# Performance work log

Hardware: AMD Instinct MI355X
Metric: run time of the kernel (lower is better)

Reference implementation:

```python
import jax, jax.numpy as jnp
import numpy as np

B, N = 16384, 20
F = 128          # n_node_features = n_neighbors_features = embed_dim
T = 100          # time_dim
E = 128          # n_edge_features
H = 2            # n_head
OUT = 128        # output_dimension
KEY_DIM = F + T + E  # 356


def setup_inputs() -> dict:
    key = jax.random.key(0)
    ks = jax.random.split(key, 24)
    s = 0.02
    inp = {
        "src_node_features": jax.random.normal(ks[0], (B, F), jnp.float32),
        "neighbors_features": jax.random.normal(ks[1], (B, N, F), jnp.float32),
        "neighbors_time_features": jax.random.normal(ks[2], (B, N, T), jnp.float32),
        "edge_features": jax.random.normal(ks[3], (B, N, E), jnp.float32),
        "neighbors_padding_mask": jax.random.randint(ks[4], (B, N), 0, 2).astype(bool),
        "weights": jax.random.uniform(ks[5], (B, N), jnp.float32),
        # transform: Linear(key_dim -> F)
        "Wt": jax.random.normal(ks[6], (F, KEY_DIM), jnp.float32) * s,
        "bt": jnp.zeros((F,), jnp.float32),
        # MultiheadAttention projections (embed_dim = kdim = vdim = F)
        "Wq": jax.random.normal(ks[7], (F, F), jnp.float32) * s,
        "bq": jnp.zeros((F,), jnp.float32),
        "Wk": jax.random.normal(ks[8], (F, F), jnp.float32) * s,
        "bk": jnp.zeros((F,), jnp.float32),
        "Wv": jax.random.normal(ks[9], (F, F), jnp.float32) * s,
        "bv": jnp.zeros((F,), jnp.float32),
        "Wo": jax.random.normal(ks[10], (F, F), jnp.float32) * s,
        "bo": jnp.zeros((F,), jnp.float32),
        # MergeLayer: fc1(query_dim + F -> F), fc2(F -> OUT)
        "W1": jax.random.normal(ks[11], (F, F + F), jnp.float32) * s,
        "b1": jnp.zeros((F,), jnp.float32),
        "W2": jax.random.normal(ks[12], (OUT, F), jnp.float32) * s,
        "b2": jnp.zeros((OUT,), jnp.float32),
    }
    return inp


def _gat_forward(src, nbr, timef, edgef, w, mask,
                 Wt, bt, Wq, bq, Wk, bk, Wv, bv, Wo, bo, W1, b1, W2, b2):
    b, f = src.shape
    dh = f // H
    scale = 1.0 / jnp.sqrt(jnp.asarray(dh, src.dtype))
    # key = transform(cat([nbr, edge, time])) * weights  -> [B,N,F]
    k_in = jnp.concatenate([nbr, edgef, timef], axis=2)
    keyv = (jnp.einsum('bnk,fk->bnf', k_in, Wt) + bt) * w[:, :, None]
    # invalid-neighborhood fixup: rows fully padded get their first slot unmasked
    invalid = mask.all(axis=1, keepdims=True)           # [B,1]
    mask = mask.at[:, 0].set(jnp.where(invalid[:, 0], False, mask[:, 0]))
    # projections (query_len = 1)
    q = (src @ Wq.T + bq).reshape(b, H, dh)             # [B,H,dh]
    k = (keyv @ Wk.T + bk).reshape(b, N, H, dh)         # [B,N,H,dh]
    v = (keyv @ Wv.T + bv).reshape(b, N, H, dh)
    scores = jnp.einsum('bhd,bnhd->bhn', q, k) * scale  # [B,H,N]
    scores = jnp.where(mask[:, None, :], -jnp.inf, scores)
    attn = jax.nn.softmax(scores, axis=-1)
    ctx = jnp.einsum('bhn,bnhd->bhd', attn, v).reshape(b, f)
    out = ctx @ Wo.T + bo                               # [B,F]
    out = jnp.where(invalid, jnp.asarray(0.0, out.dtype), out)
    out = jax.nn.relu(out)
    # MergeLayer: fc2(relu(fc1(cat([attn_out, src]))))
    hmid = jax.nn.relu(jnp.concatenate([out, src], axis=1) @ W1.T + b1)
    return hmid @ W2.T + b2


def reference(src_node_features, neighbors_features, neighbors_time_features,
              edge_features, neighbors_padding_mask, weights,
              Wt, bt, Wq, bq, Wk, bk, Wv, bv, Wo, bo, W1, b1, W2, b2):
    return _gat_forward(src_node_features, neighbors_features,
                        neighbors_time_features, edge_features, weights,
                        neighbors_padding_mask,
                        Wt, bt, Wq, bq, Wk, bk, Wv, bv, Wo, bo, W1, b1, W2, b2)
```

## Files before the change

kernel.cpp:

```cpp
#include <hip/hip_runtime.h>
#include <math.h>

#define NN 20
#define FF 128
#define TT 100
#define EE 128
#define KD 356

typedef unsigned int u32;
typedef unsigned short u16;
typedef unsigned long long u64;
typedef __attribute__((ext_vector_type(4))) float f32x4;
typedef __attribute__((ext_vector_type(8))) short s16x8;

__device__ __forceinline__ u16 f2b(float f) {
    u32 u = __float_as_uint(f);
    u32 r = u + 0x7FFFu + ((u >> 16) & 1u);
    return (u16)(r >> 16);
}
__device__ __forceinline__ float b2f(u16 h) { return __uint_as_float(((u32)h) << 16); }
__device__ __forceinline__ float blo(u32 u){ return __uint_as_float(u << 16); }
__device__ __forceinline__ float bhi(u32 u){ return __uint_as_float(u & 0xFFFF0000u); }
__device__ __forceinline__ u32 pk2(float a, float b){ return (u32)f2b(a) | ((u32)f2b(b) << 16); }


__global__ void prep_fuse(const float* __restrict__ Wt, const float* __restrict__ bt,
                          const float* __restrict__ Wk, const float* __restrict__ Wv,
                          const u32* __restrict__ maskw,
                          float* __restrict__ wkt, float* __restrict__ wvt,
                          float* __restrict__ kfb, float* __restrict__ vfb, int* __restrict__ flagp)
{
    const int blk = blockIdx.x, t = threadIdx.x;
    if (blk < KD) {
        __shared__ float col[FF];
        col[t] = Wt[t * KD + blk];
        __syncthreads();
        float ak = 0.f, av = 0.f;
        for (int j = 0; j < FF; ++j) {
            float c = col[j];
            ak = fmaf(Wk[t * FF + j], c, ak);
            av = fmaf(Wv[t * FF + j], c, av);
        }
        wkt[blk * FF + t] = ak;
        wvt[blk * FF + t] = av;
    } else if (blk == KD) {
        float ak = 0.f, av = 0.f;
        for (int j = 0; j < FF; ++j) {
            float c = bt[j];
            ak = fmaf(Wk[t * FF + j], c, ak);
            av = fmaf(Wv[t * FF + j], c, av);
        }
        kfb[t] = ak; vfb[t] = av;
    } else {
        int any = 0;
        for (int i = t; i < 8192; i += 128) any |= (maskw[i] > 1u) ? 1 : 0;
        any = __any(any) ? 1 : 0;
        __shared__ int red[2];
        if ((t & 63) == 0) red[t >> 6] = any;
        __syncthreads();
        if (t == 0) *flagp = (red[0] | red[1]) ? 1 : 0;
    }
}

__global__ void prep_pack_v4(const float* __restrict__ wkt, const float* __restrict__ wvt,
                             const float* __restrict__ Wq, const float* __restrict__ Wo,
                             const float* __restrict__ W1, const float* __restrict__ W2,
                             u16* __restrict__ kvB, u16* __restrict__ wqI, u16* __restrict__ woI,
                             u16* __restrict__ w1I, u16* __restrict__ w2I)
{
    const int id = blockIdx.x * 256 + threadIdx.x;
    if (id < 196608) {
        int chunk = id >> 9, e = id & 511;
        int ln = e >> 3, ee = e & 7;
        int kt = chunk >> 4, nb = chunk & 15;
        int k = kt * 32 + (ln >> 4) * 8 + ee;
        int n = nb * 16 + (ln & 15);
        float v = 0.f;
        if (k < KD) v = (n < FF) ? wkt[k * FF + n] : wvt[k * FF + (n - FF)];
        kvB[id] = f2b(v);
    } else if (id < 215040) {
        int e = id - 196608; int rem = e % 9216;
        int n = rem / 72, kk = rem % 72; int k = (e / 9216) * 64 + kk;
        wqI[e] = f2b(kk < 64 ? Wq[n * FF + k] : 0.f);
    } else if (id < 233472) {
        int e = id - 215040; int rem = e % 9216;
        int n = rem / 72, kk = rem % 72; int k = (e / 9216) * 64 + kk;
        woI[e] = f2b(kk < 64 ? Wo[n * FF + k] : 0.f);
    } else if (id < 270336) {
        int e = id - 233472; int rem = e % 9216;
        int n = rem / 72, kk = rem % 72; int k = (e / 9216) * 64 + kk;
        w1I[e] = f2b(kk < 64 ? W1[n * 2 * FF + k] : 0.f);
    } else if (id < 288768) {
        int e = id - 270336; int rem = e % 9216;
        int n = rem / 72, kk = rem % 72; int k = (e / 9216) * 64 + kk;
        w2I[e] = f2b(kk < 64 ? W2[n * FF + k] : 0.f);
    }
}

__device__ __forceinline__ void loadA32(const float* __restrict__ nbr,
                                        const float* __restrict__ edg,
                                        const float* __restrict__ tmf,
                                        size_t r, int g, int kt, f32x4& v0, f32x4& v1)
{
    int c0 = g * 8;
    if (kt < 4) {
        const float* p = nbr + r * 128 + kt * 32 + c0;
        v0 = *(const f32x4*)p; v1 = *(const f32x4*)(p + 4);
    } else if (kt < 8) {
        const float* p = edg + r * 128 + (kt - 4) * 32 + c0;
        v0 = *(const f32x4*)p; v1 = *(const f32x4*)(p + 4);
    } else {
        int c = (kt - 8) * 32 + c0;
        const float* p = tmf + r * 100 + c;
        v0 = (c + 3 < 100) ? *(const f32x4*)p       : (f32x4){0.f,0.f,0.f,0.f};
        v1 = (c + 7 < 100) ? *(const f32x4*)(p + 4) : (f32x4){0.f,0.f,0.f,0.f};
    }
}

__global__ __launch_bounds__(512) void kv_attn_fused2(
    const float* __restrict__ nbr, const float* __restrict__ edg, const float* __restrict__ tmf,
    const float* __restrict__ wgt, const float* __restrict__ bk, const float* __restrict__ bv,
    const u16* __restrict__ kvB, const float* __restrict__ kfb, const float* __restrict__ vfb,
    const u16* __restrict__ Qg, const void* __restrict__ maskp, const int* __restrict__ flagp,
    u16* __restrict__ ctxout, unsigned char* __restrict__ flags)
{
    __shared__ __align__(16) u16 smem[20800];
    const int tid = threadIdx.x;
    const int lane = tid & 63, wave = tid >> 6;
    const int wn = wave;
    const int Mbase = blockIdx.x * 80;
    const int Bbase = blockIdx.x * 4;
    const int kg = lane >> 4, l16 = lane & 15;

    const bool stg = tid < 320;
    const int skg = (tid >> 4) & 3;
    const int srow = (tid >> 6) * 16 + (tid & 15);
    const size_t gr = (size_t)(Mbase + srow);

    f32x4 acc[5][2] = {};

    f32x4 pa0, pa1;
    if (stg) loadA32(nbr, edg, tmf, gr, skg, 0, pa0, pa1);
    s16x8 bc0 = *(const s16x8*)(kvB + (size_t)(wn * 2 + 0) * 512 + lane * 8);
    s16x8 bc1 = *(const s16x8*)(kvB + (size_t)(wn * 2 + 1) * 512 + lane * 8);
    if (stg)
        *(uint4*)(&smem[tid * 8]) = make_uint4(pk2(pa0.x,pa0.y), pk2(pa0.z,pa0.w),
                                               pk2(pa1.x,pa1.y), pk2(pa1.z,pa1.w));
    __syncthreads();

    #pragma unroll
    for (int kt = 0; kt < 12; ++kt) {
        const u16* curA = smem + (kt & 1) * 2560;
        u16* nxtA = (u16*)smem + ((kt + 1) & 1) * 2560;

        f32x4 na0, na1; s16x8 bn0, bn1;
        if (kt < 11) {
            if (stg) loadA32(nbr, edg, tmf, gr, skg, kt + 1, na0, na1);
            bn0 = *(const s16x8*)(kvB + (size_t)((kt + 1) * 16 + wn * 2 + 0) * 512 + lane * 8);
            bn1 = *(const s16x8*)(kvB + (size_t)((kt + 1) * 16 + wn * 2 + 1) * 512 + lane * 8);
        }
        s16x8 af[5];
        #pragma unroll
        for (int mt = 0; mt < 5; ++mt)
            af[mt] = *(const s16x8*)(&curA[(mt * 4 + kg) * 128 + l16 * 8]);
        #pragma unroll
        for (int mt = 0; mt < 5; ++mt) {
            acc[mt][0] = __builtin_amdgcn_mfma_f32_16x16x32_bf16(af[mt], bc0, acc[mt][0], 0, 0, 0);
            acc[mt][1] = __builtin_amdgcn_mfma_f32_16x16x32_bf16(af[mt], bc1, acc[mt][1], 0, 0, 0);
        }
        if (kt < 11) {
            if (stg)
                *(uint4*)(&nxtA[tid * 8]) = make_uint4(pk2(na0.x,na0.y), pk2(na0.z,na0.w),
                                                       pk2(na1.x,na1.y), pk2(na1.z,na1.w));
            bc0 = bn0; bc1 = bn1;
        }
        __syncthreads();
    }

    u16* kvls = smem;
    {
        const int rg = (lane >> 4) * 4;
        #pragma unroll
        for (int mt = 0; mt < 5; ++mt) {
            const int r0 = mt * 16 + rg;
            float w4v[4];
            #pragma unroll
            for (int i = 0; i < 4; ++i) w4v[i] = wgt[Mbase + r0 + i];
            #pragma unroll
            for (int nt = 0; nt < 2; ++nt) {
                const int c = wn * 32 + nt * 16 + l16;
                const float fb = (c < FF) ? kfb[c] : vfb[c - FF];
                const float bb = (c < FF) ? bk[c]  : bv[c - FF];
                #pragma unroll
                for (int i = 0; i < 4; ++i)
                    kvls[(r0 + i) * 260 + c] = f2b(fmaf(acc[mt][nt][i] + fb, w4v[i], bb));
            }
        }
    }
    __syncthreads();

    {
        const int lb = wave >> 1, h = wave & 1;
        const int brow = Bbase + lb;
        const int flagv = *flagp;
        bool mybit = false;
        if (lane < NN) {
            if (flagv) mybit = ((const unsigned char*)maskp)[brow * NN + lane] != 0;
            else       mybit = ((const int*)maskp)[brow * NN + lane] != 0;
        }
        u64 bal = __ballot(mybit);
        u32 mb = (u32)(bal & 0xFFFFFull);
        const bool invalid = (mb == 0xFFFFFu);
        if (invalid) mb &= ~1u;
        if (h == 0 && lane == 0) flags[brow] = invalid ? 1 : 0;

        float p = 0.f;
        {
            const int n = lane & 31;
            float s = -INFINITY;
            if (lane < 32 && n < NN) {
                const u16* kr = kvls + (lb * NN + n) * 260 + h * 64;
                const u16* qr = Qg + (size_t)brow * 128 + h * 64;
                float d = 0.f;
                #pragma unroll
                for (int dc = 0; dc < 16; ++dc) {
                    uint2 kw = *(const uint2*)(kr + dc * 4);
                    uint2 qw = *(const uint2*)(qr + dc * 4);
                    d = fmaf(blo(kw.x), blo(qw.x), d);  d = fmaf(bhi(kw.x), bhi(qw.x), d);
                    d = fmaf(blo(kw.y), blo(qw.y), d);  d = fmaf(bhi(kw.y), bhi(qw.y), d);
                }
                s = ((mb >> n) & 1u) ? -INFINITY : d * 0.125f;
            }
            float mx = s;
            #pragma unroll
            for (int off = 16; off; off >>= 1) mx = fmaxf(mx, __shfl_xor(mx, off, 32));
            float e = (lane < 32 && (lane & 31) < NN) ? expf(s - mx) : 0.f;
            float sum = e;
            #pragma unroll
            for (int off = 16; off; off >>= 1) sum += __shfl_xor(sum, off, 32);
            p = (lane < 32) ? e / sum : 0.f;
        }
        float cacc = 0.f;
        #pragma unroll
        for (int n2 = 0; n2 < NN; ++n2) {
            float pn = __shfl(p, n2);
            cacc = fmaf(pn, b2f(kvls[(lb * NN + n2) * 260 + 128 + h * 64 + lane]), cacc);
        }
        ctxout[(size_t)brow * 128 + h * 64 + lane] = f2b(cacc);
    }
}

#define GM_Q 0
#define GM_O 1
#define GM_H 2
#define GM_F 3

template<int MODE>
__global__ __launch_bounds__(256) void gemm_small(
    const void* __restrict__ Asrc, const float* __restrict__ Asrc2,
    const u16* __restrict__ Bimg, const float* __restrict__ bias,
    const unsigned char* __restrict__ flags, void* __restrict__ outp)
{
    __shared__ u16 lA[64 * 72];
    __shared__ u16 lB[128 * 72];
    const int tid = threadIdx.x;
    const int Mbase = blockIdx.x * 64;
    const int lane = tid & 63, wave = tid >> 6;
    const int wm = wave >> 1, wn = wave & 1;
    const int row = tid >> 2, cg = tid & 3;

    constexpr int KTILES = (MODE == GM_H) ? 4 : 2;
    f32x4 acc[2][4] = {};
    const size_t r = (size_t)(Mbase + row);

    for (int kt = 0; kt < KTILES; ++kt) {
        if (MODE == GM_Q || (MODE == GM_H && kt >= 2)) {
            const float* ap = (MODE == GM_Q)
                ? ((const float*)Asrc + r * 128 + kt * 64 + cg * 16)
                : (Asrc2 + r * 128 + (kt - 2) * 64 + cg * 16);
            f32x4 x0 = *(const f32x4*)ap,       x1 = *(const f32x4*)(ap + 4);
            f32x4 x2 = *(const f32x4*)(ap + 8), x3 = *(const f32x4*)(ap + 12);
            *(uint4*)(&lA[row * 72 + cg * 16])     = make_uint4(pk2(x0.x,x0.y), pk2(x0.z,x0.w), pk2(x1.x,x1.y), pk2(x1.z,x1.w));
            *(uint4*)(&lA[row * 72 + cg * 16 + 8]) = make_uint4(pk2(x2.x,x2.y), pk2(x2.z,x2.w), pk2(x3.x,x3.y), pk2(x3.z,x3.w));
        } else {
            const u16* ap = (const u16*)Asrc + r * 128 + kt * 64 + cg * 16;
            *(uint4*)(&lA[row * 72 + cg * 16])     = *(const uint4*)ap;
            *(uint4*)(&lA[row * 72 + cg * 16 + 8]) = *(const uint4*)(ap + 8);
        }
        for (int c = wave; c < 18; c += 4) {
            const char* g = (const char*)Bimg + (size_t)kt * 18432 + c * 1024 + lane * 16;
            char* l = (char*)lB + c * 1024;
            __builtin_amdgcn_global_load_lds((const __attribute__((address_space(1))) u32*)g,
                                             (__attribute__((address_space(3))) u32*)l, 16, 0, 0);
        }
        __syncthreads();
        #pragma unroll
        for (int ks = 0; ks < 2; ++ks) {
            int kk = ks * 32 + (lane >> 4) * 8;
            s16x8 a[2], b[4];
            #pragma unroll
            for (int mt = 0; mt < 2; ++mt)
                a[mt] = *(const s16x8*)(&lA[(wm * 32 + mt * 16 + (lane & 15)) * 72 + kk]);
            #pragma unroll
            for (int nt = 0; nt < 4; ++nt)
                b[nt] = *(const s16x8*)(&lB[(wn * 64 + nt * 16 + (lane & 15)) * 72 + kk]);
            #pragma unroll
            for (int mt = 0; mt < 2; ++mt)
                #pragma unroll
                for (int nt = 0; nt < 4; ++nt)
                    acc[mt][nt] = __builtin_amdgcn_mfma_f32_16x16x32_bf16(a[mt], b[nt], acc[mt][nt], 0, 0, 0);
        }
        __syncthreads();
    }

    #pragma unroll
    for (int mt = 0; mt < 2; ++mt) {
        #pragma unroll
        for (int nt = 0; nt < 4; ++nt) {
            int colg = wn * 64 + nt * 16 + (lane & 15);
            float bb = bias[colg];
            #pragma unroll
            for (int i = 0; i < 4; ++i) {
                int rg = Mbase + wm * 32 + mt * 16 + (lane >> 4) * 4 + i;
                float val = acc[mt][nt][i] + bb;
                if (MODE == GM_O) { if (flags[rg]) val = 0.f; val = fmaxf(val, 0.f); }
                if (MODE == GM_H) val = fmaxf(val, 0.f);
                if (MODE == GM_F) ((float*)outp)[(size_t)rg * 128 + colg] = val;
                else              ((u16*)outp)[(size_t)rg * 128 + colg] = f2b(val);
            }
        }
    }
}


__global__ void prep_pack_r2(const float* __restrict__ wkt, const float* __restrict__ wvt,
                             const float* __restrict__ Wq, const float* __restrict__ Wo,
                             const float* __restrict__ W1, const float* __restrict__ W2,
                             u16* __restrict__ bpack, u32* __restrict__ wq2, u32* __restrict__ wo2,
                             u32* __restrict__ w12, u32* __restrict__ w22)
{
    const int id = blockIdx.x * 256 + threadIdx.x;
    if (id < 98304) {
        int kt = id >> 14;
        int o  = id & 16383;
        int n  = o >> 6;
        int kk = (o & 63) ^ ((n & 7) << 3);
        int k  = kt * 64 + kk;
        float v = 0.f;
        if (k < KD) v = (n < FF) ? wkt[k * FF + n] : wvt[k * FF + (n - FF)];
        bpack[id] = f2b(v);
    } else if (id < 106496) {
        int e = id - 98304; int j = e >> 6, tt = e & 63;
        wq2[e] = (u32)f2b(Wq[tt * FF + j]) | ((u32)f2b(Wq[(tt + 64) * FF + j]) << 16);
    } else if (id < 114688) {
        int e = id - 106496; int j = e >> 6, tt = e & 63;
        wo2[e] = (u32)f2b(Wo[tt * FF + j]) | ((u32)f2b(Wo[(tt + 64) * FF + j]) << 16);
    } else if (id < 131072) {
        int e = id - 114688; int j = e >> 6, tt = e & 63;
        w12[e] = (u32)f2b(W1[tt * 2 * FF + j]) | ((u32)f2b(W1[(tt + 64) * 2 * FF + j]) << 16);
    } else if (id < 139264) {
        int e = id - 131072; int j = e >> 6, tt = e & 63;
        w22[e] = (u32)f2b(W2[tt * FF + j]) | ((u32)f2b(W2[(tt + 64) * FF + j]) << 16);
    }
}

__global__ __launch_bounds__(512) void kv_gemm_r2(
    const float* __restrict__ nbr, const float* __restrict__ edg, const float* __restrict__ tmf,
    const float* __restrict__ wgt, const float* __restrict__ bk, const float* __restrict__ bv,
    const u16* __restrict__ bpack, const float* __restrict__ kfb, const float* __restrict__ vfb,
    u16* __restrict__ kvout)
{
    __shared__ u16 lA[128 * 64];
    __shared__ u16 lB[256 * 64];
    const int tid = threadIdx.x;
    const int Mbase = blockIdx.x * 128;
    const int lane = tid & 63, wave = tid >> 6;
    const int wm = wave >> 2, wn = wave & 3;

    f32x4 acc[4][4] = {};
    const int rq = tid >> 4;
    const int cq = tid & 15;

    for (int kt = 0; kt < 6; ++kt) {
        #pragma unroll
        for (int i = 0; i < 4; ++i) {
            int row = rq + i * 32;
            size_t r = (size_t)(Mbase + row);
            f32x4 v;
            if (kt < 2)       v = *(const f32x4*)(nbr + r * 128 + kt * 64 + cq * 4);
            else if (kt < 4)  v = *(const f32x4*)(edg + r * 128 + (kt - 2) * 64 + cq * 4);
            else if (kt == 4) v = *(const f32x4*)(tmf + r * 100 + cq * 4);
            else if (cq < 9)  v = *(const f32x4*)(tmf + r * 100 + 64 + cq * 4);
            else              v = (f32x4){0.f, 0.f, 0.f, 0.f};
            int off = row * 64 + ((cq * 4) ^ ((row & 7) << 3));
            *(uint2*)(&lA[off]) = make_uint2(pk2(v.x, v.y), pk2(v.z, v.w));
        }
        #pragma unroll
        for (int i = 0; i < 4; ++i) {
            int boff = wave * 4096 + i * 1024;
            const char* g = (const char*)bpack + (size_t)kt * 32768 + boff + lane * 16;
            char* l = (char*)lB + boff;
            __builtin_amdgcn_global_load_lds((const __attribute__((address_space(1))) u32*)g,
                                             (__attribute__((address_space(3))) u32*)l, 16, 0, 0);
        }
        __syncthreads();
        #pragma unroll
        for (int ks = 0; ks < 2; ++ks) {
            int kk = ks * 32 + (lane >> 4) * 8;
            s16x8 a[4], b[4];
            #pragma unroll
            for (int mt = 0; mt < 4; ++mt) {
                int m = wm * 64 + mt * 16 + (lane & 15);
                a[mt] = *(const s16x8*)(&lA[m * 64 + (kk ^ ((m & 7) << 3))]);
            }
            #pragma unroll
            for (int nt = 0; nt < 4; ++nt) {
                int n = wn * 64 + nt * 16 + (lane & 15);
                b[nt] = *(const s16x8*)(&lB[n * 64 + (kk ^ ((n & 7) << 3))]);
            }
            #pragma unroll
            for (int mt = 0; mt < 4; ++mt)
                #pragma unroll
                for (int nt = 0; nt < 4; ++nt)
                    acc[mt][nt] = __builtin_amdgcn_mfma_f32_16x16x32_bf16(a[mt], b[nt], acc[mt][nt], 0, 0, 0);
        }
        __syncthreads();
    }

    #pragma unroll
    for (int mt = 0; mt < 4; ++mt) {
        float w4[4];
        #pragma unroll
        for (int i = 0; i < 4; ++i)
            w4[i] = wgt[Mbase + wm * 64 + mt * 16 + (lane >> 4) * 4 + i];
        #pragma unroll
        for (int nt = 0; nt < 4; ++nt) {
            int c = wn * 64 + nt * 16 + (lane & 15);
            float fb   = (c < FF) ? kfb[c] : vfb[c - FF];
            float bias = (c < FF) ? bk[c]  : bv[c - FF];
            #pragma unroll
            for (int i = 0; i < 4; ++i) {
                int rr = Mbase + wm * 64 + mt * 16 + (lane >> 4) * 4 + i;
                float val = fmaf(acc[mt][nt][i] + fb, w4[i], bias);
                kvout[(size_t)rr * 256 + c] = f2b(val);
            }
        }
    }
}

__global__ __launch_bounds__(64) void gat_attn_r2(
    const float* __restrict__ src, const void* __restrict__ maskp,
    const float* __restrict__ bq, const float* __restrict__ bo,
    const float* __restrict__ b1, const float* __restrict__ b2,
    const u16* __restrict__ kv, const u32* __restrict__ wq2, const u32* __restrict__ wo2,
    const u32* __restrict__ w12, const u32* __restrict__ w22,
    const int* __restrict__ flagp, float* __restrict__ out)
{
    const int b = blockIdx.x, t = threadIdx.x;
    __shared__ u16 kls[NN * 132];
    __shared__ float s_src[FF], s_q[FF], s_ctx[FF], s_out[FF], s_h[FF];
    __shared__ float s_sc[2 * NN];

    const int flag = *flagp;
    bool mybit = false;
    if (t < NN) {
        if (flag) mybit = ((const unsigned char*)maskp)[b * NN + t] != 0;
        else      mybit = ((const int*)maskp)[b * NN + t] != 0;
    }
    u64 bal = __ballot(mybit);
    u32 mb = (u32)(bal & 0xFFFFFull);
    const bool invalid = (mb == 0xFFFFFu);
    if (invalid) mb &= ~1u;

    s_src[t] = src[(size_t)b * FF + t];
    s_src[t + 64] = src[(size_t)b * FF + 64 + t];

    float v0[NN], v1[NN];
    #pragma unroll
    for (int n = 0; n < NN; ++n) {
        const u16* row = kv + ((size_t)b * NN + n) * 256;
        kls[n * 132 + t]      = row[t];
        kls[n * 132 + 64 + t] = row[64 + t];
        v0[n] = b2f(row[128 + t]);
        v1[n] = b2f(row[192 + t]);
    }
    __syncthreads();

    {
        float q0 = bq[t], q1 = bq[64 + t];
        for (int j = 0; j < FF; ++j) {
            u32 u = wq2[j * 64 + t];
            float sj = s_src[j];
            q0 = fmaf(blo(u), sj, q0);
            q1 = fmaf(bhi(u), sj, q1);
        }
        s_q[t] = q0; s_q[64 + t] = q1;
    }
    __syncthreads();

    if (t < 2 * NN) {
        int h = t / NN, n = t - (t / NN) * NN;
        const u16* kr = kls + n * 132 + h * 64;
        const float* qr = s_q + h * 64;
        float s = 0.f;
        #pragma unroll
        for (int d = 0; d < 64; ++d) s = fmaf(qr[d], b2f(kr[d]), s);
        s *= 0.125f;
        s_sc[t] = ((mb >> n) & 1u) ? -INFINITY : s;
    }
    __syncthreads();
    if (t < 2) {
        float mx = -INFINITY;
        for (int n = 0; n < NN; ++n) mx = fmaxf(mx, s_sc[t * NN + n]);
        float e[NN]; float sum = 0.f;
        for (int n = 0; n < NN; ++n) { e[n] = expf(s_sc[t * NN + n] - mx); sum += e[n]; }
        float inv = 1.f / sum;
        for (int n = 0; n < NN; ++n) s_sc[t * NN + n] = e[n] * inv;
    }
    __syncthreads();

    {
        float c0 = 0.f, c1 = 0.f;
        #pragma unroll
        for (int n = 0; n < NN; ++n) {
            c0 = fmaf(s_sc[n],      v0[n], c0);
            c1 = fmaf(s_sc[NN + n], v1[n], c1);
        }
        s_ctx[t] = c0; s_ctx[64 + t] = c1;
    }
    __syncthreads();

    {
        float o0 = bo[t], o1 = bo[64 + t];
        for (int j = 0; j < FF; ++j) {
            u32 u = wo2[j * 64 + t];
            float cj = s_ctx[j];
            o0 = fmaf(blo(u), cj, o0);
            o1 = fmaf(bhi(u), cj, o1);
        }
        if (invalid) { o0 = 0.f; o1 = 0.f; }
        o0 = fmaxf(o0, 0.f); o1 = fmaxf(o1, 0.f);
        s_out[t] = o0; s_out[64 + t] = o1;
    }
    __syncthreads();

    {
        float h0 = b1[t], h1 = b1[64 + t];
        for (int j = 0; j < FF; ++j) {
            u32 u = w12[j * 64 + t];
            float xj = s_out[j];
            h0 = fmaf(blo(u), xj, h0);
            h1 = fmaf(bhi(u), xj, h1);
        }
        for (int j = 0; j < FF; ++j) {
            u32 u = w12[(FF + j) * 64 + t];
            float xj = s_src[j];
            h0 = fmaf(blo(u), xj, h0);
            h1 = fmaf(bhi(u), xj, h1);
        }
        h0 = fmaxf(h0, 0.f); h1 = fmaxf(h1, 0.f);
        s_h[t] = h0; s_h[64 + t] = h1;
    }
    __syncthreads();

    {
        float f0 = b2[t], f1 = b2[64 + t];
        for (int j = 0; j < FF; ++j) {
            u32 u = w22[j * 64 + t];
            float hj = s_h[j];
            f0 = fmaf(blo(u), hj, f0);
            f1 = fmaf(bhi(u), hj, f1);
        }
        out[(size_t)b * FF + t] = f0;
        out[(size_t)b * FF + 64 + t] = f1;
    }
}


#define FB_WKT  0
#define FB_WVT  (FB_WKT + KD*FF)
#define FB_KB   (FB_WVT + KD*FF)
#define FB_VB   (FB_KB + FF)
#define FB_WQT  (FB_VB + FF)
#define FB_WOT  (FB_WQT + FF*FF)
#define FB_W1T  (FB_WOT + FF*FF)
#define FB_W2T  (FB_W1T + 2*FF*FF)
#define FB_FLAG (FB_W2T + FF*FF)

__global__ void gat_prep_fb(const float* __restrict__ Wt, const float* __restrict__ bt,
                            const float* __restrict__ Wq, const float* __restrict__ Wk,
                            const float* __restrict__ Wv, const float* __restrict__ Wo,
                            const float* __restrict__ W1, const float* __restrict__ W2,
                            const u32* __restrict__ maskw, float* __restrict__ ws)
{
    const int blk = blockIdx.x;
    const int t = threadIdx.x;
    if (blk < KD) {
        __shared__ float col[FF];
        col[t] = Wt[t * KD + blk];
        __syncthreads();
        float ak = 0.f, av = 0.f;
        for (int j = 0; j < FF; ++j) {
            float c = col[j];
            ak = fmaf(Wk[t * FF + j], c, ak);
            av = fmaf(Wv[t * FF + j], c, av);
        }
        ws[FB_WKT + blk * FF + t] = ak;
        ws[FB_WVT + blk * FF + t] = av;
    } else if (blk == KD) {
        float ak = 0.f, av = 0.f;
        for (int j = 0; j < FF; ++j) {
            float c = bt[j];
            ak = fmaf(Wk[t * FF + j], c, ak);
            av = fmaf(Wv[t * FF + j], c, av);
        }
        ws[FB_KB + t] = ak;
        ws[FB_VB + t] = av;
    } else if (blk == KD + 1) {
        int any = 0;
        for (int i = t; i < 8192; i += 128) any |= (maskw[i] > 1u) ? 1 : 0;
        any = __any(any) ? 1 : 0;
        __shared__ int red[2];
        if ((t & 63) == 0) red[t >> 6] = any;
        __syncthreads();
        if (t == 0) ((int*)ws)[FB_FLAG] = (red[0] | red[1]) ? 1 : 0;
    } else {
        int id = (blk - (KD + 2)) * 128 + t;
        if (id < FF * FF) {
            int k = id >> 7, f = id & 127;
            ws[FB_WQT + id] = Wq[f * FF + k];
        } else if (id < 2 * FF * FF) {
            int e = id - FF * FF; int k = e >> 7, f = e & 127;
            ws[FB_WOT + e] = Wo[f * FF + k];
        } else if (id < 4 * FF * FF) {
            int e = id - 2 * FF * FF; int j = e >> 7, f = e & 127;
            ws[FB_W1T + e] = W1[f * (2 * FF) + j];
        } else if (id < 5 * FF * FF) {
            int e = id - 4 * FF * FF; int k = e >> 7, f = e & 127;
            ws[FB_W2T + e] = W2[f * FF + k];
        }
    }
}

__global__ __launch_bounds__(64) void gat_main_fb(
    const float* __restrict__ src, const float* __restrict__ nbr,
    const float* __restrict__ tmf, const float* __restrict__ edg,
    const void* __restrict__ maskp, const float* __restrict__ wgt,
    const float* __restrict__ bq, const float* __restrict__ bk,
    const float* __restrict__ bv, const float* __restrict__ bo,
    const float* __restrict__ b1, const float* __restrict__ b2,
    const float* __restrict__ ws, float* __restrict__ out)
{
    const int b = blockIdx.x;
    const int t = threadIdx.x;
    __shared__ __align__(16) float kin[KD * NN];
    __shared__ float s_src[FF], s_q[FF], s_ctx[FF], s_out[FF], s_h[FF];
    __shared__ float s_w[NN], s_sc[2 * NN];

    const int flag = ((const int*)ws)[FB_FLAG];
    bool mybit = false;
    if (t < NN) {
        if (flag) mybit = ((const unsigned char*)maskp)[b * NN + t] != 0;
        else      mybit = ((const int*)maskp)[b * NN + t] != 0;
    }
    u64 bal = __ballot(mybit);
    u32 mb = (u32)(bal & 0xFFFFFull);
    const bool invalid = (mb == 0xFFFFFu);
    if (invalid) mb &= ~1u;

    s_src[t] = src[(size_t)b * FF + t];
    s_src[t + 64] = src[(size_t)b * FF + 64 + t];
    if (t < NN) s_w[t] = wgt[(size_t)b * NN + t];

    for (int idx = t; idx < NN * FF; idx += 64) {
        int n = idx >> 7, j = idx & 127;
        kin[j * NN + n]         = nbr[((size_t)b * NN + n) * FF + j];
        kin[(128 + j) * NN + n] = edg[((size_t)b * NN + n) * EE + j];
    }
    for (int idx = t; idx < NN * TT; idx += 64) {
        int n = idx / TT, j = idx - n * TT;
        kin[(256 + j) * NN + n] = tmf[((size_t)b * NN + n) * TT + j];
    }
    __syncthreads();

    const float* wkt = ws + FB_WKT;
    const float* wvt = ws + FB_WVT;
    float ak0[NN], ak1[NN], av0[NN], av1[NN];
#pragma unroll
    for (int n = 0; n < NN; ++n) { ak0[n] = 0.f; ak1[n] = 0.f; av0[n] = 0.f; av1[n] = 0.f; }
    for (int k = 0; k < KD; ++k) {
        float wk0 = wkt[k * FF + t],      wk1 = wkt[k * FF + 64 + t];
        float wv0 = wvt[k * FF + t],      wv1 = wvt[k * FF + 64 + t];
        const float4* cp = (const float4*)(kin + k * NN);
        float4 ca = cp[0], cb = cp[1], cc = cp[2], cd = cp[3], ce = cp[4];
        const float c[NN] = { ca.x, ca.y, ca.z, ca.w,  cb.x, cb.y, cb.z, cb.w,
                              cc.x, cc.y, cc.z, cc.w,  cd.x, cd.y, cd.z, cd.w,
                              ce.x, ce.y, ce.z, ce.w };
#pragma unroll
        for (int n = 0; n < NN; ++n) {
            ak0[n] = fmaf(wk0, c[n], ak0[n]);
            ak1[n] = fmaf(wk1, c[n], ak1[n]);
            av0[n] = fmaf(wv0, c[n], av0[n]);
            av1[n] = fmaf(wv1, c[n], av1[n]);
        }
    }
    __syncthreads();

    float* kls = kin;
    float* vls = kin + NN * 129;
    {
        const float kb0 = ws[FB_KB + t], kb1 = ws[FB_KB + 64 + t];
        const float vb0 = ws[FB_VB + t], vb1 = ws[FB_VB + 64 + t];
        const float k0b = bk[t], k1b = bk[64 + t];
        const float v0b = bv[t], v1b = bv[64 + t];
#pragma unroll
        for (int n = 0; n < NN; ++n) {
            float wn = s_w[n];
            kls[n * 129 + t]      = fmaf(wn, ak0[n] + kb0, k0b);
            kls[n * 129 + 64 + t] = fmaf(wn, ak1[n] + kb1, k1b);
            vls[n * 129 + t]      = fmaf(wn, av0[n] + vb0, v0b);
            vls[n * 129 + 64 + t] = fmaf(wn, av1[n] + vb1, v1b);
        }
    }
    {
        const float* wqT = ws + FB_WQT;
        float q0 = bq[t], q1 = bq[64 + t];
        for (int j = 0; j < FF; ++j) {
            float sj = s_src[j];
            q0 = fmaf(wqT[j * FF + t], sj, q0);
            q1 = fmaf(wqT[j * FF + 64 + t], sj, q1);
        }
        s_q[t] = q0; s_q[64 + t] = q1;
    }
    __syncthreads();

    if (t < 2 * NN) {
        int h = t / NN, n = t - (t / NN) * NN;
        const float* kr = kls + n * 129 + h * 64;
        const float* qr = s_q + h * 64;
        float s = 0.f;
#pragma unroll
        for (int d = 0; d < 64; ++d) s = fmaf(qr[d], kr[d], s);
        s *= 0.125f;
        s_sc[t] = ((mb >> n) & 1u) ? -INFINITY : s;
    }
    __syncthreads();
    if (t < 2) {
        float mx = -INFINITY;
        for (int n = 0; n < NN; ++n) mx = fmaxf(mx, s_sc[t * NN + n]);
        float e[NN]; float sum = 0.f;
        for (int n = 0; n < NN; ++n) { e[n] = expf(s_sc[t * NN + n] - mx); sum += e[n]; }
        float inv = 1.f / sum;
        for (int n = 0; n < NN; ++n) s_sc[t * NN + n] = e[n] * inv;
    }
    __syncthreads();

    {
        float c0 = 0.f, c1 = 0.f;
#pragma unroll
        for (int n = 0; n < NN; ++n) {
            c0 = fmaf(s_sc[n],      vls[n * 129 + t],      c0);
            c1 = fmaf(s_sc[NN + n], vls[n * 129 + 64 + t], c1);
        }
        s_ctx[t] = c0; s_ctx[64 + t] = c1;
    }
    __syncthreads();

    {
        const float* woT = ws + FB_WOT;
        float o0 = bo[t], o1 = bo[64 + t];
        for (int j = 0; j < FF; ++j) {
            float cj = s_ctx[j];
            o0 = fmaf(woT[j * FF + t], cj, o0);
            o1 = fmaf(woT[j * FF + 64 + t], cj, o1);
        }
        if (invalid) { o0 = 0.f; o1 = 0.f; }
        o0 = fmaxf(o0, 0.f); o1 = fmaxf(o1, 0.f);
        s_out[t] = o0; s_out[64 + t] = o1;
    }
    __syncthreads();

    {
        const float* w1T = ws + FB_W1T;
        float h0 = b1[t], h1 = b1[64 + t];
        for (int j = 0; j < FF; ++j) {
            float xj = s_out[j];
            h0 = fmaf(w1T[j * FF + t], xj, h0);
            h1 = fmaf(w1T[j * FF + 64 + t], xj, h1);
        }
        for (int j = 0; j < FF; ++j) {
            float xj = s_src[j];
            h0 = fmaf(w1T[(FF + j) * FF + t], xj, h0);
            h1 = fmaf(w1T[(FF + j) * FF + 64 + t], xj, h1);
        }
        h0 = fmaxf(h0, 0.f); h1 = fmaxf(h1, 0.f);
        s_h[t] = h0; s_h[64 + t] = h1;
    }
    __syncthreads();

    {
        const float* w2T = ws + FB_W2T;
        float f0 = b2[t], f1 = b2[64 + t];
        for (int j = 0; j < FF; ++j) {
            float hj = s_h[j];
            f0 = fmaf(w2T[j * FF + t], hj, f0);
            f1 = fmaf(w2T[j * FF + 64 + t], hj, f1);
        }
        out[(size_t)b * FF + t] = f0;
        out[(size_t)b * FF + 64 + t] = f1;
    }
}


extern "C" void kernel_launch(void* const* d_in, const int* in_sizes, int n_in,
                              void* d_out, int out_size, void* d_ws, size_t ws_size,
                              hipStream_t stream)
{
    const float* src = (const float*)d_in[0];
    const float* nbr = (const float*)d_in[1];
    const float* tmf = (const float*)d_in[2];
    const float* edg = (const float*)d_in[3];
    const void*  msk = d_in[4];
    const float* wgt = (const float*)d_in[5];
    const float* Wt  = (const float*)d_in[6];
    const float* bt  = (const float*)d_in[7];
    const float* Wq  = (const float*)d_in[8];
    const float* bq  = (const float*)d_in[9];
    const float* Wk  = (const float*)d_in[10];
    const float* bk  = (const float*)d_in[11];
    const float* Wv  = (const float*)d_in[12];
    const float* bv  = (const float*)d_in[13];
    const float* Wo  = (const float*)d_in[14];
    const float* bo  = (const float*)d_in[15];
    const float* W1  = (const float*)d_in[16];
    const float* b1  = (const float*)d_in[17];
    const float* W2  = (const float*)d_in[18];
    const float* b2  = (const float*)d_in[19];

    const int B = in_sizes[0] / FF;
    const size_t M = (size_t)B * NN;

    size_t o1 = 0;
    size_t t1_qa   = o1; o1 += (size_t)B * 256;
    size_t t1_ch   = o1; o1 += (size_t)B * 256;
    size_t t1_kvB  = o1; o1 += 393216;
    size_t t1_wqI  = o1; o1 += 36864;
    size_t t1_woI  = o1; o1 += 36864;
    size_t t1_w1I  = o1; o1 += 73728;
    size_t t1_w2I  = o1; o1 += 36864;
    size_t t1_wkt  = o1; o1 += (size_t)KD * FF * 4;
    size_t t1_wvt  = o1; o1 += (size_t)KD * FF * 4;
    size_t t1_kfb  = o1; o1 += 512;
    size_t t1_vfb  = o1; o1 += 512;
    size_t t1_flg  = o1; o1 += (size_t)B;
    o1 = (o1 + 255) & ~(size_t)255;
    size_t t1_flag = o1; o1 += 64;
    const size_t need1 = o1;

    size_t o2 = 0;
    size_t t2_kv    = o2; o2 += M * 512;
    size_t t2_bpack = o2; o2 += 98304ull * 2;
    size_t t2_wkt   = o2; o2 += (size_t)KD * FF * 4;
    size_t t2_wvt   = o2; o2 += (size_t)KD * FF * 4;
    size_t t2_kfb   = o2; o2 += 512;
    size_t t2_vfb   = o2; o2 += 512;
    size_t t2_wq2   = o2; o2 += 32768;
    size_t t2_wo2   = o2; o2 += 32768;
    size_t t2_w12   = o2; o2 += 65536;
    size_t t2_w22   = o2; o2 += 32768;
    size_t t2_flag  = o2; o2 += 64;
    const size_t need2 = o2;

    char* w = (char*)d_ws;

    if (ws_size >= need1 && (B % 64) == 0) {
        u16*   qa    = (u16*)(w + t1_qa);
        u16*   ch    = (u16*)(w + t1_ch);
        u16*   kvB   = (u16*)(w + t1_kvB);
        u16*   wqI   = (u16*)(w + t1_wqI);
        u16*   woI   = (u16*)(w + t1_woI);
        u16*   w1I   = (u16*)(w + t1_w1I);
        u16*   w2I   = (u16*)(w + t1_w2I);
        float* wktp  = (float*)(w + t1_wkt);
        float* wvtp  = (float*)(w + t1_wvt);
        float* kfb   = (float*)(w + t1_kfb);
        float* vfb   = (float*)(w + t1_vfb);
        unsigned char* flg = (unsigned char*)(w + t1_flg);
        int*   flagp = (int*)(w + t1_flag);

        prep_fuse<<<dim3(KD + 2), dim3(128), 0, stream>>>(Wt, bt, Wk, Wv,
            (const u32*)msk, wktp, wvtp, kfb, vfb, flagp);
        prep_pack_v4<<<dim3(1128), dim3(256), 0, stream>>>(wktp, wvtp, Wq, Wo, W1, W2,
            kvB, wqI, woI, w1I, w2I);
        gemm_small<GM_Q><<<dim3(B / 64), dim3(256), 0, stream>>>(
            (const void*)src, nullptr, wqI, bq, nullptr, (void*)qa);
        kv_attn_fused2<<<dim3(B / 4), dim3(512), 0, stream>>>(
            nbr, edg, tmf, wgt, bk, bv, kvB, kfb, vfb, qa, msk, flagp, ch, flg);
        gemm_small<GM_O><<<dim3(B / 64), dim3(256), 0, stream>>>(
            (const void*)ch, nullptr, woI, bo, flg, (void*)qa);
        gemm_small<GM_H><<<dim3(B / 64), dim3(256), 0, stream>>>(
            (const void*)qa, src, w1I, b1, nullptr, (void*)ch);
        gemm_small<GM_F><<<dim3(B / 64), dim3(256), 0, stream>>>(
            (const void*)ch, nullptr, w2I, b2, nullptr, d_out);
    } else if (ws_size >= need2 && (M % 128) == 0) {
        u16*   kvp   = (u16*)(w + t2_kv);
        u16*   bpack = (u16*)(w + t2_bpack);
        float* wktp  = (float*)(w + t2_wkt);
        float* wvtp  = (float*)(w + t2_wvt);
        float* kfb   = (float*)(w + t2_kfb);
        float* vfb   = (float*)(w + t2_vfb);
        u32*   wq2   = (u32*)(w + t2_wq2);
        u32*   wo2   = (u32*)(w + t2_wo2);
        u32*   w12   = (u32*)(w + t2_w12);
        u32*   w22   = (u32*)(w + t2_w22);
        int*   flagp = (int*)(w + t2_flag);

        prep_fuse<<<dim3(KD + 2), dim3(128), 0, stream>>>(Wt, bt, Wk, Wv,
            (const u32*)msk, wktp, wvtp, kfb, vfb, flagp);
        prep_pack_r2<<<dim3(544), dim3(256), 0, stream>>>(wktp, wvtp, Wq, Wo, W1, W2,
            bpack, wq2, wo2, w12, w22);
        kv_gemm_r2<<<dim3((int)(M / 128)), dim3(512), 0, stream>>>(
            nbr, edg, tmf, wgt, bk, bv, bpack, kfb, vfb, kvp);
        gat_attn_r2<<<dim3(B), dim3(64), 0, stream>>>(
            src, msk, bq, bo, b1, b2, kvp, wq2, wo2, w12, w22, flagp, (float*)d_out);
    } else {
        float* ws = (float*)d_ws;
        gat_prep_fb<<<dim3(KD + 2 + 640), dim3(128), 0, stream>>>(
            Wt, bt, Wq, Wk, Wv, Wo, W1, W2, (const u32*)msk, ws);
        gat_main_fb<<<dim3(B), dim3(64), 0, stream>>>(
            src, nbr, tmf, edg, msk, wgt, bq, bk, bv, bo, b1, b2, ws, (float*)d_out);
    }
}
```

Measured before the change: 205.7 us.

## Restructure fused KV-attention kernel to load A directly into registers per wave

Replaces the LDS double-buffered A staging with direct global loads converted to bf16 in registers, with each of 5 waves owning 32 rows and all 256 K/V output columns. The block now handles 8 batch rows instead of 4. V stays in registers while K goes to LDS, and V reuses the same LDS after the softmax. The goal is to remove the per-k-step barriers and LDS traffic and to reuse each A fragment across more B columns. The cost is many more B-fragment loads per wave, since the full weight matrix is read by every wave, and heavy register pressure from 32 accumulators under launch bounds of 2 blocks.

```diff
diff --git a/kernel.cpp b/kernel.cpp
--- a/kernel.cpp
+++ b/kernel.cpp
@@ -12,6 +12,7 @@
 typedef unsigned long long u64;
 typedef __attribute__((ext_vector_type(4))) float f32x4;
 typedef __attribute__((ext_vector_type(8))) short s16x8;
+typedef __attribute__((ext_vector_type(4))) u32 u32x4;
 
 __device__ __forceinline__ u16 f2b(float f) {
     u32 u = __float_as_uint(f);
@@ -22,6 +23,9 @@
 __device__ __forceinline__ float blo(u32 u){ return __uint_as_float(u << 16); }
 __device__ __forceinline__ float bhi(u32 u){ return __uint_as_float(u & 0xFFFF0000u); }
 __device__ __forceinline__ u32 pk2(float a, float b){ return (u32)f2b(a) | ((u32)f2b(b) << 16); }
+__device__ __forceinline__ u32 cvtpk(float a, float b){
+    u32 d; asm("v_cvt_pk_bf16_f32 %0, %1, %2" : "=v"(d) : "v"(a), "v"(b)); return d;
+}
 
 
 __global__ void prep_fuse(const float* __restrict__ Wt, const float* __restrict__ bt,
@@ -97,129 +101,115 @@
     }
 }
 
-__device__ __forceinline__ void loadA32(const float* __restrict__ nbr,
-                                        const float* __restrict__ edg,
-                                        const float* __restrict__ tmf,
-                                        size_t r, int g, int kt, f32x4& v0, f32x4& v1)
-{
-    int c0 = g * 8;
-    if (kt < 4) {
-        const float* p = nbr + r * 128 + kt * 32 + c0;
-        v0 = *(const f32x4*)p; v1 = *(const f32x4*)(p + 4);
-    } else if (kt < 8) {
-        const float* p = edg + r * 128 + (kt - 4) * 32 + c0;
-        v0 = *(const f32x4*)p; v1 = *(const f32x4*)(p + 4);
-    } else {
-        int c = (kt - 8) * 32 + c0;
-        const float* p = tmf + r * 100 + c;
-        v0 = (c + 3 < 100) ? *(const f32x4*)p       : (f32x4){0.f,0.f,0.f,0.f};
-        v1 = (c + 7 < 100) ? *(const f32x4*)(p + 4) : (f32x4){0.f,0.f,0.f,0.f};
-    }
-}
-
-__global__ __launch_bounds__(512) void kv_attn_fused2(
+__global__ __launch_bounds__(320, 2) void kv_attn_fused6(
     const float* __restrict__ nbr, const float* __restrict__ edg, const float* __restrict__ tmf,
     const float* __restrict__ wgt, const float* __restrict__ bk, const float* __restrict__ bv,
     const u16* __restrict__ kvB, const float* __restrict__ kfb, const float* __restrict__ vfb,
     const u16* __restrict__ Qg, const void* __restrict__ maskp, const int* __restrict__ flagp,
     u16* __restrict__ ctxout, unsigned char* __restrict__ flags)
 {
-    __shared__ __align__(16) u16 smem[20800];
+    __shared__ u16 kls[160 * 132];
+    __shared__ float p_lds[320];
+
     const int tid = threadIdx.x;
     const int lane = tid & 63, wave = tid >> 6;
-    const int wn = wave;
-    const int Mbase = blockIdx.x * 80;
-    const int Bbase = blockIdx.x * 4;
     const int kg = lane >> 4, l16 = lane & 15;
-
-    const bool stg = tid < 320;
-    const int skg = (tid >> 4) & 3;
-    const int srow = (tid >> 6) * 16 + (tid & 15);
-    const size_t gr = (size_t)(Mbase + srow);
-
-    f32x4 acc[5][2] = {};
-
-    f32x4 pa0, pa1;
-    if (stg) loadA32(nbr, edg, tmf, gr, skg, 0, pa0, pa1);
-    s16x8 bc0 = *(const s16x8*)(kvB + (size_t)(wn * 2 + 0) * 512 + lane * 8);
-    s16x8 bc1 = *(const s16x8*)(kvB + (size_t)(wn * 2 + 1) * 512 + lane * 8);
-    if (stg)
-        *(uint4*)(&smem[tid * 8]) = make_uint4(pk2(pa0.x,pa0.y), pk2(pa0.z,pa0.w),
-                                               pk2(pa1.x,pa1.y), pk2(pa1.z,pa1.w));
-    __syncthreads();
-
+    const int Mbase = blockIdx.x * 160;
+    const int Bbase = blockIdx.x * 8;
+
+    f32x4 acc[2][16] = {};
+
+    #define LOADA(KT, ROW, LO, HI) do {                                                   \
+        if ((KT) < 4)       { const float* p_ = nbr + (size_t)(ROW) * 128 + (KT) * 32 + kg * 8;        \
+                              LO = *(const f32x4*)p_; HI = *(const f32x4*)(p_ + 4); }     \
+        else if ((KT) < 8)  { const float* p_ = edg + (size_t)(ROW) * 128 + ((KT) - 4) * 32 + kg * 8;  \
+                              LO = *(const f32x4*)p_; HI = *(const f32x4*)(p_ + 4); }     \
+        else if ((KT) < 11) { const float* p_ = tmf + (size_t)(ROW) * 100 + ((KT) - 8) * 32 + kg * 8;  \
+                              LO = *(const f32x4*)p_; HI = *(const f32x4*)(p_ + 4); }     \
+        else { LO = (f32x4){0.f,0.f,0.f,0.f}; HI = LO;                                    \
+               if (kg == 0) LO = *(const f32x4*)(tmf + (size_t)(ROW) * 100 + 96); }       \
+    } while (0)
+
+    #define GITER(KT) do {                                                                \
+        s16x8 af[2];                                                                      \
+        _Pragma("unroll")                                                                 \
+        for (int mt = 0; mt < 2; ++mt) {                                                  \
+            size_t row = (size_t)(Mbase + wave * 32 + mt * 16 + l16);                     \
+            f32x4 lo, hi;                                                                 \
+            LOADA(KT, row, lo, hi);                                                       \
+            u32x4 q;                                                                      \
+            q.x = cvtpk(lo.x, lo.y); q.y = cvtpk(lo.z, lo.w);                             \
+            q.z = cvtpk(hi.x, hi.y); q.w = cvtpk(hi.z, hi.w);                             \
+            af[mt] = __builtin_bit_cast(s16x8, q);                                        \
+        }                                                                                 \
+        _Pragma("unroll")                                                                 \
+        for (int g = 0; g < 2; ++g) {                                                     \
+            s16x8 bf[8];                                                                  \
+            _Pragma("unroll")                                                             \
+            for (int j = 0; j < 8; ++j)                                                   \
+                bf[j] = *(const s16x8*)(kvB + (size_t)((KT) * 16 + g * 8 + j) * 512 + lane * 8); \
+            _Pragma("unroll")                                                             \
+            for (int mt = 0; mt < 2; ++mt)                                                \
+                _Pragma("unroll")                                                         \
+                for (int j = 0; j < 8; ++j)                                               \
+                    acc[mt][g * 8 + j] = __builtin_amdgcn_mfma_f32_16x16x32_bf16(         \
+                        af[mt], bf[j], acc[mt][g * 8 + j], 0, 0, 0);                      \
+        }                                                                                 \
+    } while (0)
+
+    GITER(0); GITER(1); GITER(2);  GITER(3);
+    GITER(4); GITER(5); GITER(6);  GITER(7);
+    GITER(8); GITER(9); GITER(10); GITER(11);
+    #undef GITER
+    #undef LOADA
+
+    const int rg4 = (lane >> 4) * 4;
     #pragma unroll
-    for (int kt = 0; kt < 12; ++kt) {
-        const u16* curA = smem + (kt & 1) * 2560;
-        u16* nxtA = (u16*)smem + ((kt + 1) & 1) * 2560;
-
-        f32x4 na0, na1; s16x8 bn0, bn1;
-        if (kt < 11) {
-            if (stg) loadA32(nbr, edg, tmf, gr, skg, kt + 1, na0, na1);
-            bn0 = *(const s16x8*)(kvB + (size_t)((kt + 1) * 16 + wn * 2 + 0) * 512 + lane * 8);
-            bn1 = *(const s16x8*)(kvB + (size_t)((kt + 1) * 16 + wn * 2 + 1) * 512 + lane * 8);
-        }
-        s16x8 af[5];
-        #pragma unroll
-        for (int mt = 0; mt < 5; ++mt)
-            af[mt] = *(const s16x8*)(&curA[(mt * 4 + kg) * 128 + l16 * 8]);
-        #pragma unroll
-        for (int mt = 0; mt < 5; ++mt) {
-            acc[mt][0] = __builtin_amdgcn_mfma_f32_16x16x32_bf16(af[mt], bc0, acc[mt][0], 0, 0, 0);
-            acc[mt][1] = __builtin_amdgcn_mfma_f32_16x16x32_bf16(af[mt], bc1, acc[mt][1], 0, 0, 0);
-        }
-        if (kt < 11) {
-            if (stg)
-                *(uint4*)(&nxtA[tid * 8]) = make_uint4(pk2(na0.x,na0.y), pk2(na0.z,na0.w),
-                                                       pk2(na1.x,na1.y), pk2(na1.z,na1.w));
-            bc0 = bn0; bc1 = bn1;
-        }
-        __syncthreads();
-    }
-
-    u16* kvls = smem;
-    {
-        const int rg = (lane >> 4) * 4;
-        #pragma unroll
-        for (int mt = 0; mt < 5; ++mt) {
-            const int r0 = mt * 16 + rg;
-            float w4v[4];
-            #pragma unroll
-            for (int i = 0; i < 4; ++i) w4v[i] = wgt[Mbase + r0 + i];
-            #pragma unroll
-            for (int nt = 0; nt < 2; ++nt) {
-                const int c = wn * 32 + nt * 16 + l16;
-                const float fb = (c < FF) ? kfb[c] : vfb[c - FF];
-                const float bb = (c < FF) ? bk[c]  : bv[c - FF];
-                #pragma unroll
-                for (int i = 0; i < 4; ++i)
-                    kvls[(r0 + i) * 260 + c] = f2b(fmaf(acc[mt][nt][i] + fb, w4v[i], bb));
-            }
-        }
-    }
-    __syncthreads();
-
-    {
-        const int lb = wave >> 1, h = wave & 1;
-        const int brow = Bbase + lb;
+    for (int mt = 0; mt < 2; ++mt) {
+        const int lr0 = wave * 32 + mt * 16 + rg4;
+        float w4v[4];
+        #pragma unroll
+        for (int i = 0; i < 4; ++i) w4v[i] = wgt[Mbase + lr0 + i];
+        #pragma unroll
+        for (int nb = 0; nb < 8; ++nb) {
+            const int c = nb * 16 + l16;
+            const float fb = kfb[c], bb = bk[c];
+            #pragma unroll
+            for (int i = 0; i < 4; ++i)
+                kls[(lr0 + i) * 132 + c] = f2b(fmaf(acc[mt][nb][i] + fb, w4v[i], bb));
+        }
+        #pragma unroll
+        for (int nb = 8; nb < 16; ++nb) {
+            const int c = (nb - 8) * 16 + l16;
+            const float fb = vfb[c], bb = bv[c];
+            #pragma unroll
+            for (int i = 0; i < 4; ++i)
+                acc[mt][nb][i] = fmaf(acc[mt][nb][i] + fb, w4v[i], bb);
+        }
+    }
+    __syncthreads();
+
+    if (tid < 256) {
+        const int u = tid >> 5;
+        const int n = tid & 31;
+        const int brow = Bbase + u;
         const int flagv = *flagp;
         bool mybit = false;
-        if (lane < NN) {
-            if (flagv) mybit = ((const unsigned char*)maskp)[brow * NN + lane] != 0;
-            else       mybit = ((const int*)maskp)[brow * NN + lane] != 0;
+        if (n < NN) {
+            if (flagv) mybit = ((const unsigned char*)maskp)[brow * NN + n] != 0;
+            else       mybit = ((const int*)maskp)[brow * NN + n] != 0;
         }
         u64 bal = __ballot(mybit);
-        u32 mb = (u32)(bal & 0xFFFFFull);
+        u32 mb = (u32)((bal >> (lane & 32)) & 0xFFFFFull);
         const bool invalid = (mb == 0xFFFFFu);
         if (invalid) mb &= ~1u;
-        if (h == 0 && lane == 0) flags[brow] = invalid ? 1 : 0;
-
-        float p = 0.f;
-        {
-            const int n = lane & 31;
+        if (n == 0) flags[brow] = invalid ? 1 : 0;
+
+        #pragma unroll
+        for (int h = 0; h < 2; ++h) {
             float s = -INFINITY;
-            if (lane < 32 && n < NN) {
-                const u16* kr = kvls + (lb * NN + n) * 260 + h * 64;
+            if (n < NN) {
+                const u16* kr = kls + (u * NN + n) * 132 + h * 64;
                 const u16* qr = Qg + (size_t)brow * 128 + h * 64;
                 float d = 0.f;
                 #pragma unroll
@@ -234,19 +224,44 @@
             float mx = s;
             #pragma unroll
             for (int off = 16; off; off >>= 1) mx = fmaxf(mx, __shfl_xor(mx, off, 32));
-            float e = (lane < 32 && (lane & 31) < NN) ? expf(s - mx) : 0.f;
+            float e = (n < NN) ? expf(s - mx) : 0.f;
             float sum = e;
             #pragma unroll
             for (int off = 16; off; off >>= 1) sum += __shfl_xor(sum, off, 32);
-            p = (lane < 32) ? e / sum : 0.f;
-        }
-        float cacc = 0.f;
-        #pragma unroll
-        for (int n2 = 0; n2 < NN; ++n2) {
-            float pn = __shfl(p, n2);
-            cacc = fmaf(pn, b2f(kvls[(lb * NN + n2) * 260 + 128 + h * 64 + lane]), cacc);
-        }
-        ctxout[(size_t)brow * 128 + h * 64 + lane] = f2b(cacc);
+            if (n < NN) p_lds[(u * 2 + h) * NN + n] = e / sum;
+        }
+    }
+    __syncthreads();
+
+    #pragma unroll
+    for (int mt = 0; mt < 2; ++mt) {
+        const int lr0 = wave * 32 + mt * 16 + rg4;
+        #pragma unroll
+        for (int nb = 8; nb < 16; ++nb) {
+            const int c = (nb - 8) * 16 + l16;
+            #pragma unroll
+            for (int i = 0; i < 4; ++i)
+                kls[(lr0 + i) * 132 + c] = f2b(acc[mt][nb][i]);
+        }
+    }
+    __syncthreads();
+
+    if (tid < 256) {
+        const int u = tid >> 5;
+        const int d32 = tid & 31;
+        const int brow = Bbase + u;
+        #pragma unroll
+        for (int rep = 0; rep < 4; ++rep) {
+            const int d = d32 + rep * 32;
+            const int h = d >> 6;
+            float cacc = 0.f;
+            #pragma unroll
+            for (int n2 = 0; n2 < NN; ++n2) {
+                float pn = p_lds[(u * 2 + h) * NN + n2];
+                cacc = fmaf(pn, b2f(kls[(u * NN + n2) * 132 + d]), cacc);
+            }
+            ctxout[(size_t)brow * 128 + d] = f2b(cacc);
+        }
     }
 }
 
@@ -894,7 +909,7 @@
             kvB, wqI, woI, w1I, w2I);
         gemm_small<GM_Q><<<dim3(B / 64), dim3(256), 0, stream>>>(
             (const void*)src, nullptr, wqI, bq, nullptr, (void*)qa);
-        kv_attn_fused2<<<dim3(B / 4), dim3(512), 0, stream>>>(
+        kv_attn_fused6<<<dim3(B / 8), dim3(320), 0, stream>>>(
             nbr, edg, tmf, wgt, bk, bv, kvB, kfb, vfb, qa, msk, flagp, ch, flg);
         gemm_small<GM_O><<<dim3(B / 64), dim3(256), 0, stream>>>(
             (const void*)ch, nullptr, woI, bo, flg, (void*)qa);
```

New measurement: 319.8 us. 1.55x slower.
